# Kernel tuning notes

Hardware: AMD Instinct MI355X
Metric: run time of the kernel (lower is better)

The kernel has to match this reference:

```python
import jax, jax.numpy as jnp
import numpy as np

NEG_SLOPE = 0.01  # torch F.leaky_relu default used in the DGL GAT-style layer


def grat_layer(h, src, dst, W, a, n_nodes):
    """One GRAT (GAT-style) layer.
    h: [N, d_in], src/dst: [E] int, W: [d_in, d_out], a: [2*d_out] (attn_fc weight
    on concat [z_src || z_dst]). Returns [N, d_out].
    """
    d_out = W.shape[1]
    z = h @ W                                   # [N, d_out]
    # attention logits per edge: a^T [z_src || z_dst]
    s_src = z @ a[:d_out]                       # [N]
    s_dst = z @ a[d_out:]                       # [N]
    e = jax.nn.leaky_relu(s_src[src] + s_dst[dst], NEG_SLOPE)  # [E]
    # numerically stable softmax over incoming edges of each dst node
    m = jax.ops.segment_max(e, dst, num_segments=n_nodes)      # [N]
    m = jnp.where(jnp.isfinite(m), m, 0.0)      # nodes with no in-edges
    w = jnp.exp(e - m[dst])                     # [E]
    denom = jax.ops.segment_sum(w, dst, num_segments=n_nodes)  # [N]
    alpha = w / jnp.maximum(denom, 1e-9)[dst]   # [E]
    # weighted scatter-aggregate of source features into dst
    out = jax.ops.segment_sum(alpha[:, None] * z[src], dst, num_segments=n_nodes)
    return out                                  # [N, d_out]


def setup_inputs() -> dict:
    key = jax.random.key(0)
    ks = jax.random.split(key, 10)
    N, E = 100000, 1600000
    IN, H1, H2, OUT = 128, 32, 32, 1
    feature = jax.random.normal(ks[0], (N, IN), dtype=jnp.float32)
    src = jax.random.randint(ks[1], (E,), 0, N, dtype=jnp.int32)
    dst = jax.random.randint(ks[2], (E,), 0, N, dtype=jnp.int32)
    s = 0.1
    W1 = jax.random.normal(ks[3], (IN, H1), dtype=jnp.float32) * s
    a1 = jax.random.normal(ks[4], (2 * H1,), dtype=jnp.float32) * s
    W2 = jax.random.normal(ks[5], (H1, H2), dtype=jnp.float32) * s
    a2 = jax.random.normal(ks[6], (2 * H2,), dtype=jnp.float32) * s
    W3 = jax.random.normal(ks[7], (H2, OUT), dtype=jnp.float32) * s
    a3 = jax.random.normal(ks[8], (2 * OUT,), dtype=jnp.float32) * s
    return {"feature": feature, "src": src, "dst": dst,
            "W1": W1, "a1": a1, "W2": W2, "a2": a2, "W3": W3, "a3": a3}


def reference(feature, src, dst, W1, a1, W2, a2, W3, a3):
    n = feature.shape[0]
    h = jax.nn.relu(grat_layer(feature, src, dst, W1, a1, n))
    h = jax.nn.relu(grat_layer(h, src, dst, W2, a2, n))
    h = grat_layer(h, src, dst, W3, a3, n)
    return jax.nn.sigmoid(h)                    # [N, 1]
```

## Files before the change

### kernel.cpp

```cpp
#include <hip/hip_runtime.h>
#include <hip/hip_bf16.h>
#include <cstdint>
#include <cstddef>

#define NEG_SLOPE 0.01f

static __device__ __forceinline__ unsigned short f2bf(float f) {
    __hip_bfloat16 b = __float2bfloat16(f);
    return *(unsigned short*)&b;
}


__global__ __launch_bounds__(128) void gemm1_kernel(
    const float* __restrict__ h, const float* __restrict__ W,
    const float* __restrict__ a, unsigned short* __restrict__ zb,
    float* __restrict__ s_src, float* __restrict__ s_dst, int N)
{
    __shared__ float Wl[128 * 32];
    int tid = threadIdx.x;
    int rowBase = blockIdx.x * 64;

    {
        const float4* W4 = (const float4*)W;
        float4* Wl4 = (float4*)Wl;
        for (int i = tid; i < 1024; i += 128) Wl4[i] = W4[i];
    }
    __syncthreads();

    int wv   = tid >> 6;
    int lane = tid & 63;
    int g    = lane >> 3;
    int l8   = lane & 7;
    int r0   = wv * 32 + g * 4;
    int col4 = l8 * 4;

    float acc[4][4];
#pragma unroll
    for (int i = 0; i < 4; i++)
#pragma unroll
        for (int c = 0; c < 4; c++) acc[i][c] = 0.f;

    const float4* h4  = (const float4*)h;
    const float4* Wl4 = (const float4*)Wl;

    size_t rowOff[4];
#pragma unroll
    for (int i = 0; i < 4; i++) {
        int r = rowBase + r0 + i;
        rowOff[i] = (size_t)((r < N) ? r : (N - 1)) * 32;
    }

#pragma unroll 2
    for (int kq = 0; kq < 32; kq++) {
        float4 w0 = Wl4[(kq * 4 + 0) * 8 + l8];
        float4 w1 = Wl4[(kq * 4 + 1) * 8 + l8];
        float4 w2 = Wl4[(kq * 4 + 2) * 8 + l8];
        float4 w3 = Wl4[(kq * 4 + 3) * 8 + l8];
#pragma unroll
        for (int i = 0; i < 4; i++) {
            float4 hv = h4[rowOff[i] + kq];
            acc[i][0] += hv.x * w0.x; acc[i][1] += hv.x * w0.y;
            acc[i][2] += hv.x * w0.z; acc[i][3] += hv.x * w0.w;
            acc[i][0] += hv.y * w1.x; acc[i][1] += hv.y * w1.y;
            acc[i][2] += hv.y * w1.z; acc[i][3] += hv.y * w1.w;
            acc[i][0] += hv.z * w2.x; acc[i][1] += hv.z * w2.y;
            acc[i][2] += hv.z * w2.z; acc[i][3] += hv.z * w2.w;
            acc[i][0] += hv.w * w3.x; acc[i][1] += hv.w * w3.y;
            acc[i][2] += hv.w * w3.z; acc[i][3] += hv.w * w3.w;
        }
    }

    float4 alo = ((const float4*)a)[l8];
    float4 ahi = ((const float4*)a)[8 + l8];
#pragma unroll
    for (int i = 0; i < 4; i++) {
        int row = rowBase + r0 + i;
        if (row < N) {
            ushort4 zv4 = make_ushort4(f2bf(acc[i][0]), f2bf(acc[i][1]),
                                       f2bf(acc[i][2]), f2bf(acc[i][3]));
            *(ushort4*)&zb[(size_t)row * 32 + col4] = zv4;
            float ps = acc[i][0] * alo.x + acc[i][1] * alo.y + acc[i][2] * alo.z + acc[i][3] * alo.w;
            float pd = acc[i][0] * ahi.x + acc[i][1] * ahi.y + acc[i][2] * ahi.z + acc[i][3] * ahi.w;
            ps += __shfl_xor(ps, 1, 64); ps += __shfl_xor(ps, 2, 64); ps += __shfl_xor(ps, 4, 64);
            pd += __shfl_xor(pd, 1, 64); pd += __shfl_xor(pd, 2, 64); pd += __shfl_xor(pd, 4, 64);
            if (l8 == 0) { s_src[row] = ps; s_dst[row] = pd; }
        }
    }
}


#define TILE_E 4096
#define NB_MAX 512

__global__ __launch_bounds__(256) void csr_hist_kernel(
    const int* __restrict__ dst, int* __restrict__ counts,
    int E, int TB, int NB)
{
    __shared__ int hist[NB_MAX];
    int tid = threadIdx.x;
    int t = blockIdx.x;
    for (int b = tid; b < NB; b += 256) hist[b] = 0;
    __syncthreads();
    int base = t * TILE_E;
    for (int i = tid; i < TILE_E; i += 256) {
        int k = base + i;
        if (k < E) atomicAdd(&hist[dst[k] >> 8], 1);
    }
    __syncthreads();
    for (int b = tid; b < NB; b += 256) counts[b * TB + t] = hist[b];
}

__global__ __launch_bounds__(256) void scan1_kernel(
    const int* __restrict__ vals, int* __restrict__ incl,
    int* __restrict__ blockSums, int M)
{
    __shared__ int tmp[256];
    int tid = threadIdx.x;
    int i = blockIdx.x * 256 + tid;
    int v = (i < M) ? vals[i] : 0;
    tmp[tid] = v;
    __syncthreads();
#pragma unroll
    for (int off = 1; off < 256; off <<= 1) {
        int t = (tid >= off) ? tmp[tid - off] : 0;
        __syncthreads();
        tmp[tid] += t;
        __syncthreads();
    }
    if (i < M) incl[i] = tmp[tid];
    if (tid == 255) blockSums[blockIdx.x] = tmp[255];
}

__global__ __launch_bounds__(1024) void scan2_kernel(int* __restrict__ blockSums, int nb)
{
    __shared__ int tmp[1024];
    int tid = threadIdx.x;
    int v = (tid < nb) ? blockSums[tid] : 0;
    tmp[tid] = v;
    __syncthreads();
#pragma unroll
    for (int off = 1; off < 1024; off <<= 1) {
        int t = (tid >= off) ? tmp[tid - off] : 0;
        __syncthreads();
        tmp[tid] += t;
        __syncthreads();
    }
    if (tid < nb) blockSums[tid] = tmp[tid] - v;
}

__global__ __launch_bounds__(256) void scan3_kernel(
    const int* __restrict__ vals, const int* __restrict__ blockSums,
    int* __restrict__ cscan, int M, int E)
{
    int i = blockIdx.x * 256 + threadIdx.x;
    if (i < M) {
        cscan[i] = cscan[i] - vals[i] + blockSums[i >> 8];
    }
    if (i == 0) cscan[M] = E;
}

__global__ __launch_bounds__(256) void csr_scatter_kernel(
    const int* __restrict__ src, const int* __restrict__ dst,
    const int* __restrict__ cscan, int* __restrict__ ebuf,
    int E, int TB, int NB)
{
    __shared__ int baseB[NB_MAX];
    __shared__ int cur[NB_MAX];
    int tid = threadIdx.x;
    int t = blockIdx.x;
    for (int b = tid; b < NB; b += 256) {
        baseB[b] = cscan[b * TB + t];
        cur[b] = 0;
    }
    __syncthreads();
    int base = t * TILE_E;
    for (int i = tid; i < TILE_E; i += 256) {
        int k = base + i;
        if (k < E) {
            int d = dst[k], s = src[k];
            int b = d >> 8;
            int r = atomicAdd(&cur[b], 1);
            ebuf[baseB[b] + r] = (s << 8) | (d & 255);
        }
    }
}

__global__ __launch_bounds__(256) void csr_bucket_kernel(
    const int* __restrict__ ebuf, const int* __restrict__ cscan,
    int* __restrict__ csr_src, int* __restrict__ offsets,
    int N, int E, int TB)
{
    __shared__ int eb[8192];
    __shared__ int hist[256];
    __shared__ int loff[256];
    __shared__ int tmp[256];
    int tid = threadIdx.x;
    int b = blockIdx.x;

    int beg = cscan[b * TB];
    int endv = cscan[(b + 1) * TB];
    int cnt = endv - beg;
    int first = b << 8;

    hist[tid] = 0;
    __syncthreads();

    bool inLds = (cnt <= 8192);
    for (int i = tid; i < cnt; i += 256) {
        int v = ebuf[beg + i];
        if (inLds) eb[i] = v;
        atomicAdd(&hist[v & 255], 1);
    }
    __syncthreads();

    int hv = hist[tid];
    tmp[tid] = hv;
    __syncthreads();
#pragma unroll
    for (int off = 1; off < 256; off <<= 1) {
        int t = (tid >= off) ? tmp[tid - off] : 0;
        __syncthreads();
        tmp[tid] += t;
        __syncthreads();
    }
    loff[tid] = tmp[tid] - hv;
    __syncthreads();

    if (first + tid < N) offsets[first + tid] = beg + loff[tid];
    if (b == 0 && tid == 0) offsets[N] = E;

    hist[tid] = 0;
    __syncthreads();

    for (int i = tid; i < cnt; i += 256) {
        int v = inLds ? eb[i] : ebuf[beg + i];
        int d8 = v & 255;
        int r = atomicAdd(&hist[d8], 1);
        csr_src[beg + loff[d8] + r] = v >> 8;
    }
}


#define AGG32_CORE(S_SRC, S_DST, ZB)                                          \
    int beg = offsets[node], end = offsets[node + 1];                         \
    int deg = end - beg;                                                      \
    float sd = (S_DST)[node];                                                 \
    int q  = lane >> 3;                                                       \
    int c4 = (lane & 7) * 4;                                                  \
    float4 o4 = make_float4(0.f, 0.f, 0.f, 0.f);                              \
    float rden;                                                               \
    if (deg <= 128) {                                                         \
        int   sreg[4];                                                        \
        float ev[4];                                                          \
        int nIter = (deg + 31) >> 5;                                          \
        float m = -3.0e38f;                                                   \
        _Pragma("unroll 4")                                                   \
        for (int it = 0; it < nIter; ++it) {                                  \
            int p = beg + it * 32 + lane;                                     \
            float e = -3.0e38f;                                               \
            int s = 0;                                                        \
            if (p < end) {                                                    \
                s = csr_src[p];                                               \
                e = (S_SRC)[s] + sd;                                          \
                e = (e > 0.f) ? e : NEG_SLOPE * e;                            \
            }                                                                 \
            sreg[it] = s;                                                     \
            ev[it] = e;                                                       \
            m = fmaxf(m, e);                                                  \
        }                                                                     \
        _Pragma("unroll")                                                     \
        for (int off = 16; off > 0; off >>= 1)                                \
            m = fmaxf(m, __shfl_xor(m, off, 32));                             \
        float l = 0.f;                                                        \
        _Pragma("unroll 4")                                                   \
        for (int it = 0; it < nIter; ++it) {                                  \
            int p = beg + it * 32 + lane;                                     \
            float w = (p < end) ? __expf(ev[it] - m) : 0.f;                   \
            ws[it * 32 + lane] = make_float2(w, __int_as_float(sreg[it]));    \
            l += w;                                                           \
        }                                                                     \
        _Pragma("unroll")                                                     \
        for (int off = 16; off > 0; off >>= 1) l += __shfl_xor(l, off, 32);   \
        rden = 1.f / fmaxf(l, 1e-9f);                                         \
        int degP = (deg + 3) & ~3;                                            \
        int p = 0;                                                            \
        for (; p + 16 <= degP; p += 16) {                                     \
            float2 a0 = ws[p +      q], a1 = ws[p + 4  + q];                  \
            float2 a2 = ws[p + 8  + q], a3 = ws[p + 12 + q];                  \
            uint2 u0 = *(const uint2*)((ZB) + (unsigned)(__float_as_int(a0.y) * 32 + c4)); \
            uint2 u1 = *(const uint2*)((ZB) + (unsigned)(__float_as_int(a1.y) * 32 + c4)); \
            uint2 u2 = *(const uint2*)((ZB) + (unsigned)(__float_as_int(a2.y) * 32 + c4)); \
            uint2 u3 = *(const uint2*)((ZB) + (unsigned)(__float_as_int(a3.y) * 32 + c4)); \
            o4.x += a0.x * __uint_as_float(u0.x << 16);                       \
            o4.y += a0.x * __uint_as_float(u0.x & 0xffff0000u);               \
            o4.z += a0.x * __uint_as_float(u0.y << 16);                       \
            o4.w += a0.x * __uint_as_float(u0.y & 0xffff0000u);               \
            o4.x += a1.x * __uint_as_float(u1.x << 16);                       \
            o4.y += a1.x * __uint_as_float(u1.x & 0xffff0000u);               \
            o4.z += a1.x * __uint_as_float(u1.y << 16);                       \
            o4.w += a1.x * __uint_as_float(u1.y & 0xffff0000u);               \
            o4.x += a2.x * __uint_as_float(u2.x << 16);                       \
            o4.y += a2.x * __uint_as_float(u2.x & 0xffff0000u);               \
            o4.z += a2.x * __uint_as_float(u2.y << 16);                       \
            o4.w += a2.x * __uint_as_float(u2.y & 0xffff0000u);               \
            o4.x += a3.x * __uint_as_float(u3.x << 16);                       \
            o4.y += a3.x * __uint_as_float(u3.x & 0xffff0000u);               \
            o4.z += a3.x * __uint_as_float(u3.y << 16);                       \
            o4.w += a3.x * __uint_as_float(u3.y & 0xffff0000u);               \
        }                                                                     \
        for (; p < degP; p += 4) {                                            \
            float2 aa = ws[p + q];                                            \
            uint2 u = *(const uint2*)((ZB) + (unsigned)(__float_as_int(aa.y) * 32 + c4)); \
            o4.x += aa.x * __uint_as_float(u.x << 16);                        \
            o4.y += aa.x * __uint_as_float(u.x & 0xffff0000u);                \
            o4.z += aa.x * __uint_as_float(u.y << 16);                        \
            o4.w += aa.x * __uint_as_float(u.y & 0xffff0000u);                \
        }                                                                     \
    } else {                                                                  \
        float m = -3.0e38f;                                                   \
        for (int p = beg + lane; p < end; p += 32) {                          \
            float e = (S_SRC)[csr_src[p]] + sd;                               \
            e = (e > 0.f) ? e : NEG_SLOPE * e;                                \
            m = fmaxf(m, e);                                                  \
        }                                                                     \
        _Pragma("unroll")                                                     \
        for (int off = 16; off > 0; off >>= 1)                                \
            m = fmaxf(m, __shfl_xor(m, off, 32));                             \
        float l = 0.f;                                                        \
        for (int p = beg + lane; p < end; p += 32) {                          \
            float e = (S_SRC)[csr_src[p]] + sd;                               \
            e = (e > 0.f) ? e : NEG_SLOPE * e;                                \
            l += __expf(e - m);                                               \
        }                                                                     \
        _Pragma("unroll")                                                     \
        for (int off = 16; off > 0; off >>= 1) l += __shfl_xor(l, off, 32);   \
        rden = 1.f / fmaxf(l, 1e-9f);                                         \
        for (int p = 0; p < deg; p += 4) {                                    \
            int idx = p + q;                                                  \
            int valid = (idx < deg);                                          \
            int s = csr_src[beg + (valid ? idx : deg - 1)];                   \
            float e = (S_SRC)[s] + sd;                                        \
            e = (e > 0.f) ? e : NEG_SLOPE * e;                                \
            float w = valid ? __expf(e - m) : 0.f;                            \
            uint2 u = *(const uint2*)((ZB) + (unsigned)(s * 32 + c4));        \
            o4.x += w * __uint_as_float(u.x << 16);                           \
            o4.y += w * __uint_as_float(u.x & 0xffff0000u);                   \
            o4.z += w * __uint_as_float(u.y << 16);                           \
            o4.w += w * __uint_as_float(u.y & 0xffff0000u);                   \
        }                                                                     \
    }                                                                         \
    o4.x += __shfl_xor(o4.x, 8, 32);                                          \
    o4.y += __shfl_xor(o4.y, 8, 32);                                          \
    o4.z += __shfl_xor(o4.z, 8, 32);                                          \
    o4.w += __shfl_xor(o4.w, 8, 32);                                          \
    o4.x += __shfl_xor(o4.x, 16, 32);                                         \
    o4.y += __shfl_xor(o4.y, 16, 32);                                         \
    o4.z += __shfl_xor(o4.z, 16, 32);                                         \
    o4.w += __shfl_xor(o4.w, 16, 32);                                         \
    float4 vv4;                                                               \
    vv4.x = fmaxf(o4.x * rden, 0.f);                                          \
    vv4.y = fmaxf(o4.y * rden, 0.f);                                          \
    vv4.z = fmaxf(o4.z * rden, 0.f);                                          \
    vv4.w = fmaxf(o4.w * rden, 0.f);

__global__ __launch_bounds__(256) void agg32_l1_kernel(
    const int* __restrict__ offsets, const int* __restrict__ csr_src,
    const float* __restrict__ s_src1, const float* __restrict__ s_dst1,
    const unsigned short* __restrict__ zb1,
    const float* __restrict__ W2, const float* __restrict__ a2,
    unsigned short* __restrict__ zb2,
    float* __restrict__ s_src2, float* __restrict__ s_dst2, int N)
{
    __shared__ float W2l[32 * 32];
    __shared__ float2 wsbuf[8 * 128];
    __shared__ float hl[8 * 32];
    int tid = threadIdx.x;
    for (int i = tid; i < 1024; i += 256) W2l[i] = W2[i];
    __syncthreads();

    int g    = tid >> 5;
    int lane = tid & 31;
    int node = blockIdx.x * 8 + g;
    if (node >= N) return;
    float2* ws = &wsbuf[g * 128];

    AGG32_CORE(s_src1, s_dst1, zb1)

    if (q == 0) *(float4*)&hl[g * 32 + c4] = vv4;
    const float4* hb4 = (const float4*)&hl[g * 32];
    float acc2 = 0.f;
#pragma unroll
    for (int c = 0; c < 8; ++c) {
        float4 hv = hb4[c];
        acc2 += hv.x * W2l[(c * 4 + 0) * 32 + lane];
        acc2 += hv.y * W2l[(c * 4 + 1) * 32 + lane];
        acc2 += hv.z * W2l[(c * 4 + 2) * 32 + lane];
        acc2 += hv.w * W2l[(c * 4 + 3) * 32 + lane];
    }

    zb2[(size_t)node * 32 + lane] = f2bf(acc2);
    float ps = acc2 * a2[lane];
    float pd = acc2 * a2[32 + lane];
#pragma unroll
    for (int off = 16; off > 0; off >>= 1) {
        ps += __shfl_xor(ps, off, 32);
        pd += __shfl_xor(pd, off, 32);
    }
    if (lane == 0) { s_src2[node] = ps; s_dst2[node] = pd; }
}

__global__ __launch_bounds__(256) void agg32_l2_kernel(
    const int* __restrict__ offsets, const int* __restrict__ csr_src,
    const float* __restrict__ s_src2, const float* __restrict__ s_dst2,
    const unsigned short* __restrict__ zb2,
    const float* __restrict__ W3, const float* __restrict__ a3,
    float2* __restrict__ zs, float* __restrict__ s_dst3, int N)
{
    __shared__ float2 wsbuf[8 * 128];
    int tid  = threadIdx.x;
    int g    = tid >> 5;
    int lane = tid & 31;
    int node = blockIdx.x * 8 + g;
    if (node >= N) return;
    float2* ws = &wsbuf[g * 128];

    AGG32_CORE(s_src2, s_dst2, zb2)

    float4 w3q = ((const float4*)W3)[lane & 7];
    float t = vv4.x * w3q.x + vv4.y * w3q.y + vv4.z * w3q.z + vv4.w * w3q.w;
    t += __shfl_xor(t, 1, 32);
    t += __shfl_xor(t, 2, 32);
    t += __shfl_xor(t, 4, 32);
    if (lane == 0) {
        zs[node] = make_float2(t, t * a3[0]);
        s_dst3[node] = t * a3[1];
    }
}

__global__ __launch_bounds__(256) void agg1_fused_kernel(
    const int* __restrict__ offsets, const int* __restrict__ csr_src,
    const float2* __restrict__ zs, const float* __restrict__ s_dst,
    float* __restrict__ out, int N)
{
    int node = blockIdx.x * 8 + (threadIdx.x >> 5);
    int lane = threadIdx.x & 31;
    if (node >= N) return;

    int beg = offsets[node], end = offsets[node + 1];
    int deg = end - beg;
    float sd = s_dst[node];

    if (deg <= 128) {
        float ev[4], zv[4];
        int nIter = (deg + 31) >> 5;
        float m = -3.0e38f;
#pragma unroll 4
        for (int it = 0; it < nIter; ++it) {
            int p = beg + it * 32 + lane;
            float e = -3.0e38f, zz = 0.f;
            if (p < end) {
                float2 v2 = zs[csr_src[p]];
                zz = v2.x;
                e = v2.y + sd;
                e = (e > 0.f) ? e : NEG_SLOPE * e;
            }
            ev[it] = e; zv[it] = zz;
            m = fmaxf(m, e);
        }
#pragma unroll
        for (int off = 16; off > 0; off >>= 1) m = fmaxf(m, __shfl_xor(m, off, 32));
        float l = 0.f, o = 0.f;
#pragma unroll 4
        for (int it = 0; it < nIter; ++it) {
            int p = beg + it * 32 + lane;
            float w = (p < end) ? __expf(ev[it] - m) : 0.f;
            l += w;
            o += w * zv[it];
        }
#pragma unroll
        for (int off = 16; off > 0; off >>= 1) {
            l += __shfl_xor(l, off, 32);
            o += __shfl_xor(o, off, 32);
        }
        if (lane == 0) {
            float v = o / fmaxf(l, 1e-9f);
            out[node] = 1.f / (1.f + __expf(-v));
        }
    } else {
        float m = -3.0e38f;
        for (int p = beg + lane; p < end; p += 32) {
            float e = zs[csr_src[p]].y + sd;
            e = (e > 0.f) ? e : NEG_SLOPE * e;
            m = fmaxf(m, e);
        }
#pragma unroll
        for (int off = 16; off > 0; off >>= 1) m = fmaxf(m, __shfl_xor(m, off, 32));
        float l = 0.f, o = 0.f;
        for (int p = beg + lane; p < end; p += 32) {
            float2 v2 = zs[csr_src[p]];
            float e = v2.y + sd;
            e = (e > 0.f) ? e : NEG_SLOPE * e;
            float w = __expf(e - m);
            l += w; o += w * v2.x;
        }
#pragma unroll
        for (int off = 16; off > 0; off >>= 1) {
            l += __shfl_xor(l, off, 32);
            o += __shfl_xor(o, off, 32);
        }
        if (lane == 0) {
            float v = o / fmaxf(l, 1e-9f);
            out[node] = 1.f / (1.f + __expf(-v));
        }
    }
}


extern "C" void kernel_launch(void* const* d_in, const int* in_sizes, int n_in,
                              void* d_out, int out_size, void* d_ws, size_t ws_size,
                              hipStream_t stream)
{
    const float* feature = (const float*)d_in[0];
    const int*   src     = (const int*)d_in[1];
    const int*   dst     = (const int*)d_in[2];
    const float* W1      = (const float*)d_in[3];
    const float* a1      = (const float*)d_in[4];
    const float* W2      = (const float*)d_in[5];
    const float* a2      = (const float*)d_in[6];
    const float* W3      = (const float*)d_in[7];
    const float* a3      = (const float*)d_in[8];
    float* out = (float*)d_out;

    const int N = in_sizes[0] / 128;
    const int E = in_sizes[1];

    const int TB = (E + TILE_E - 1) / TILE_E;
    const int NB = (N + 255) >> 8;
    const int M  = NB * TB;

    char* p = (char*)d_ws;
    unsigned short* zb1 = (unsigned short*)p;  p += (size_t)N * 32 * sizeof(unsigned short);
    unsigned short* zb2 = (unsigned short*)p;  p += (size_t)N * 32 * sizeof(unsigned short);
    float* zs32    = (float*)p;  p += (size_t)N * 2 * sizeof(float);
    float* s_src1  = (float*)p;  p += (size_t)N * sizeof(float);
    float* s_dst1  = (float*)p;  p += (size_t)N * sizeof(float);
    float* s_src2  = (float*)p;  p += (size_t)N * sizeof(float);
    float* s_dst2  = (float*)p;  p += (size_t)N * sizeof(float);
    float* s_dst3  = (float*)p;  p += (size_t)N * sizeof(float);
    int*   offsets = (int*)p;    p += ((size_t)N + 1) * sizeof(int);
    int*   counts  = (int*)p;    p += ((size_t)M + 1) * sizeof(int);
    int*   cscan   = (int*)p;    p += ((size_t)M + 1) * sizeof(int);
    int*   blockSums = (int*)p;  p += 1024 * sizeof(int);
    int*   ebuf    = (int*)p;    p += (size_t)E * sizeof(int);
    int*   csr_src = (int*)p;    p += (size_t)E * sizeof(int);

    const int nodeBlocks8  = (N + 7) / 8;
    const int gemmBlocks64 = (N + 63) / 64;
    const int scanBlocksM  = (M + 255) / 256;

    hipLaunchKernelGGL(csr_hist_kernel, dim3(TB), dim3(256), 0, stream,
                       dst, counts, E, TB, NB);
    hipLaunchKernelGGL(scan1_kernel, dim3(scanBlocksM), dim3(256), 0, stream,
                       counts, cscan, blockSums, M);
    hipLaunchKernelGGL(scan2_kernel, dim3(1), dim3(1024), 0, stream,
                       blockSums, scanBlocksM);
    hipLaunchKernelGGL(scan3_kernel, dim3(scanBlocksM), dim3(256), 0, stream,
                       counts, blockSums, cscan, M, E);
    hipLaunchKernelGGL(csr_scatter_kernel, dim3(TB), dim3(256), 0, stream,
                       src, dst, cscan, ebuf, E, TB, NB);
    hipLaunchKernelGGL(csr_bucket_kernel, dim3(NB), dim3(256), 0, stream,
                       ebuf, cscan, csr_src, offsets, N, E, TB);

    hipLaunchKernelGGL(gemm1_kernel, dim3(gemmBlocks64), dim3(128), 0, stream,
                       feature, W1, a1, zb1, s_src1, s_dst1, N);
    hipLaunchKernelGGL(agg32_l1_kernel, dim3(nodeBlocks8), dim3(256), 0, stream,
                       offsets, csr_src, s_src1, s_dst1, zb1, W2, a2,
                       zb2, s_src2, s_dst2, N);

    float2* zs = (float2*)zs32;
    hipLaunchKernelGGL(agg32_l2_kernel, dim3(nodeBlocks8), dim3(256), 0, stream,
                       offsets, csr_src, s_src2, s_dst2, zb2, W3, a3,
                       zs, s_dst3, N);

    hipLaunchKernelGGL(agg1_fused_kernel, dim3(nodeBlocks8), dim3(256), 0, stream,
                       offsets, csr_src, zs, s_dst3, out, N);
}
```

Baseline: 256.3 us.

## Fold block-sum scan into scan3, precompute W2·a2, and pre-shift gather offsets

Drops the single-block scan2 kernel; each scan3 block now reduces the preceding block sums itself, which removes one launch but adds redundant reads. In layer-1 aggregation, W2·a2 is precomputed per block so the layer-2 attention scores come from the pre-transform features with a short shuffle reduction. W2 columns are held in registers rather than read from LDS. Source indices are pre-shifted to byte offsets to simplify gather address arithmetic. Together these trim launch overhead and per-node ALU/LDS work, at the cost of higher register pressure.

```diff
diff --git a/kernel.cpp b/kernel.cpp
--- a/kernel.cpp
+++ b/kernel.cpp
@@ -131,31 +131,25 @@
     if (tid == 255) blockSums[blockIdx.x] = tmp[255];
 }
 
-__global__ __launch_bounds__(1024) void scan2_kernel(int* __restrict__ blockSums, int nb)
-{
-    __shared__ int tmp[1024];
-    int tid = threadIdx.x;
-    int v = (tid < nb) ? blockSums[tid] : 0;
-    tmp[tid] = v;
-    __syncthreads();
-#pragma unroll
-    for (int off = 1; off < 1024; off <<= 1) {
-        int t = (tid >= off) ? tmp[tid - off] : 0;
-        __syncthreads();
-        tmp[tid] += t;
-        __syncthreads();
-    }
-    if (tid < nb) blockSums[tid] = tmp[tid] - v;
-}
-
 __global__ __launch_bounds__(256) void scan3_kernel(
     const int* __restrict__ vals, const int* __restrict__ blockSums,
     int* __restrict__ cscan, int M, int E)
 {
-    int i = blockIdx.x * 256 + threadIdx.x;
-    if (i < M) {
-        cscan[i] = cscan[i] - vals[i] + blockSums[i >> 8];
-    }
+    __shared__ int red[256];
+    int tid = threadIdx.x;
+    int bid = blockIdx.x;
+    int partial = 0;
+    for (int j = tid; j < bid; j += 256) partial += blockSums[j];
+    red[tid] = partial;
+    __syncthreads();
+#pragma unroll
+    for (int off = 128; off > 0; off >>= 1) {
+        if (tid < off) red[tid] += red[tid + off];
+        __syncthreads();
+    }
+    int prefix = red[0];
+    int i = bid * 256 + tid;
+    if (i < M) cscan[i] = cscan[i] - vals[i] + prefix;
     if (i == 0) cscan[M] = E;
 }
 
@@ -247,6 +241,8 @@
     float sd = (S_DST)[node];                                                 \
     int q  = lane >> 3;                                                       \
     int c4 = (lane & 7) * 4;                                                  \
+    unsigned cb = (unsigned)(lane & 7) * 8u;                                  \
+    const char* zbc = (const char*)(ZB);                                      \
     float4 o4 = make_float4(0.f, 0.f, 0.f, 0.f);                              \
     float rden;                                                               \
     if (deg <= 128) {                                                         \
@@ -264,7 +260,7 @@
                 e = (S_SRC)[s] + sd;                                          \
                 e = (e > 0.f) ? e : NEG_SLOPE * e;                            \
             }                                                                 \
-            sreg[it] = s;                                                     \
+            sreg[it] = s << 6;                                                \
             ev[it] = e;                                                       \
             m = fmaxf(m, e);                                                  \
         }                                                                     \
@@ -287,10 +283,10 @@
         for (; p + 16 <= degP; p += 16) {                                     \
             float2 a0 = ws[p +      q], a1 = ws[p + 4  + q];                  \
             float2 a2 = ws[p + 8  + q], a3 = ws[p + 12 + q];                  \
-            uint2 u0 = *(const uint2*)((ZB) + (unsigned)(__float_as_int(a0.y) * 32 + c4)); \
-            uint2 u1 = *(const uint2*)((ZB) + (unsigned)(__float_as_int(a1.y) * 32 + c4)); \
-            uint2 u2 = *(const uint2*)((ZB) + (unsigned)(__float_as_int(a2.y) * 32 + c4)); \
-            uint2 u3 = *(const uint2*)((ZB) + (unsigned)(__float_as_int(a3.y) * 32 + c4)); \
+            uint2 u0 = *(const uint2*)(zbc + (cb + (unsigned)__float_as_int(a0.y))); \
+            uint2 u1 = *(const uint2*)(zbc + (cb + (unsigned)__float_as_int(a1.y))); \
+            uint2 u2 = *(const uint2*)(zbc + (cb + (unsigned)__float_as_int(a2.y))); \
+            uint2 u3 = *(const uint2*)(zbc + (cb + (unsigned)__float_as_int(a3.y))); \
             o4.x += a0.x * __uint_as_float(u0.x << 16);                       \
             o4.y += a0.x * __uint_as_float(u0.x & 0xffff0000u);               \
             o4.z += a0.x * __uint_as_float(u0.y << 16);                       \
@@ -310,7 +306,7 @@
         }                                                                     \
         for (; p < degP; p += 4) {                                            \
             float2 aa = ws[p + q];                                            \
-            uint2 u = *(const uint2*)((ZB) + (unsigned)(__float_as_int(aa.y) * 32 + c4)); \
+            uint2 u = *(const uint2*)(zbc + (cb + (unsigned)__float_as_int(aa.y))); \
             o4.x += aa.x * __uint_as_float(u.x << 16);                        \
             o4.y += aa.x * __uint_as_float(u.x & 0xffff0000u);                \
             o4.z += aa.x * __uint_as_float(u.y << 16);                        \
@@ -342,7 +338,7 @@
             float e = (S_SRC)[s] + sd;                                        \
             e = (e > 0.f) ? e : NEG_SLOPE * e;                                \
             float w = valid ? __expf(e - m) : 0.f;                            \
-            uint2 u = *(const uint2*)((ZB) + (unsigned)(s * 32 + c4));        \
+            uint2 u = *(const uint2*)(zbc + (cb + ((unsigned)s << 6)));       \
             o4.x += w * __uint_as_float(u.x << 16);                           \
             o4.y += w * __uint_as_float(u.x & 0xffff0000u);                   \
             o4.z += w * __uint_as_float(u.y << 16);                           \
@@ -374,38 +370,53 @@
     __shared__ float W2l[32 * 32];
     __shared__ float2 wsbuf[8 * 128];
     __shared__ float hl[8 * 32];
+    __shared__ float w2a[64];
     int tid = threadIdx.x;
     for (int i = tid; i < 1024; i += 256) W2l[i] = W2[i];
     __syncthreads();
 
+    if (tid < 64) {
+        const float* av = a2 + (tid >> 5) * 32;
+        int k = tid & 31;
+        float sacc = 0.f;
+#pragma unroll
+        for (int j = 0; j < 32; ++j) sacc += W2l[k * 32 + j] * av[j];
+        w2a[tid] = sacc;
+    }
+    int lane = tid & 31;
+    float w2r[32];
+#pragma unroll
+    for (int k = 0; k < 32; ++k) w2r[k] = W2l[k * 32 + lane];
+    __syncthreads();
+
     int g    = tid >> 5;
-    int lane = tid & 31;
     int node = blockIdx.x * 8 + g;
     if (node >= N) return;
     float2* ws = &wsbuf[g * 128];
 
     AGG32_CORE(s_src1, s_dst1, zb1)
 
+    float4 waS = *(const float4*)&w2a[c4];
+    float4 waD = *(const float4*)&w2a[32 + c4];
+    float ps = vv4.x * waS.x + vv4.y * waS.y + vv4.z * waS.z + vv4.w * waS.w;
+    float pd = vv4.x * waD.x + vv4.y * waD.y + vv4.z * waD.z + vv4.w * waD.w;
+    ps += __shfl_xor(ps, 1, 32); pd += __shfl_xor(pd, 1, 32);
+    ps += __shfl_xor(ps, 2, 32); pd += __shfl_xor(pd, 2, 32);
+    ps += __shfl_xor(ps, 4, 32); pd += __shfl_xor(pd, 4, 32);
+
     if (q == 0) *(float4*)&hl[g * 32 + c4] = vv4;
     const float4* hb4 = (const float4*)&hl[g * 32];
     float acc2 = 0.f;
 #pragma unroll
     for (int c = 0; c < 8; ++c) {
         float4 hv = hb4[c];
-        acc2 += hv.x * W2l[(c * 4 + 0) * 32 + lane];
-        acc2 += hv.y * W2l[(c * 4 + 1) * 32 + lane];
-        acc2 += hv.z * W2l[(c * 4 + 2) * 32 + lane];
-        acc2 += hv.w * W2l[(c * 4 + 3) * 32 + lane];
+        acc2 += hv.x * w2r[c * 4 + 0];
+        acc2 += hv.y * w2r[c * 4 + 1];
+        acc2 += hv.z * w2r[c * 4 + 2];
+        acc2 += hv.w * w2r[c * 4 + 3];
     }
 
     zb2[(size_t)node * 32 + lane] = f2bf(acc2);
-    float ps = acc2 * a2[lane];
-    float pd = acc2 * a2[32 + lane];
-#pragma unroll
-    for (int off = 16; off > 0; off >>= 1) {
-        ps += __shfl_xor(ps, off, 32);
-        pd += __shfl_xor(pd, off, 32);
-    }
     if (lane == 0) { s_src2[node] = ps; s_dst2[node] = pd; }
 }
 
@@ -562,8 +573,6 @@
                        dst, counts, E, TB, NB);
     hipLaunchKernelGGL(scan1_kernel, dim3(scanBlocksM), dim3(256), 0, stream,
                        counts, cscan, blockSums, M);
-    hipLaunchKernelGGL(scan2_kernel, dim3(1), dim3(1024), 0, stream,
-                       blockSums, scanBlocksM);
     hipLaunchKernelGGL(scan3_kernel, dim3(scanBlocksM), dim3(256), 0, stream,
                        counts, blockSums, cscan, M, E);
     hipLaunchKernelGGL(csr_scatter_kernel, dim3(TB), dim3(256), 0, stream,
```

Measured after the change: 281.6 us. +9.9%, slower.
